# Performance work log

Hardware: AMD Instinct MI355X
Metric: run time of the kernel (lower is better)

Reference implementation:

```python
import jax, jax.numpy as jnp
import numpy as np

NC, ND = 100000, 100000
E, L = 500000, 100000
HID, OUT = 128, 64
NH, HD = 4, 32
NL = 2


def setup_inputs() -> dict:
    key = jax.random.key(0)
    ks = jax.random.split(key, 16)
    f = jnp.float32
    s_lin = 1.0 / np.sqrt(HID)
    s_rel = 1.0 / np.sqrt(HD)
    return {
        "emb_C": jax.random.normal(ks[0], (NC, HID), f) * 0.1,
        "emb_D": jax.random.normal(ks[1], (ND, HID), f) * 0.1,
        "kW": jax.random.normal(ks[2], (NL, 2, HID, HID), f) * s_lin,
        "kb": jnp.zeros((NL, 2, HID), f),
        "qW": jax.random.normal(ks[3], (NL, 2, HID, HID), f) * s_lin,
        "qb": jnp.zeros((NL, 2, HID), f),
        "vW": jax.random.normal(ks[4], (NL, 2, HID, HID), f) * s_lin,
        "vb": jnp.zeros((NL, 2, HID), f),
        "aW": jax.random.normal(ks[5], (NL, 2, HID, HID), f) * s_lin,
        "ab": jnp.zeros((NL, 2, HID), f),
        "skip": jnp.ones((NL, 2), f),
        "arel": jax.random.normal(ks[6], (NL, 2, NH, HD, HD), f) * s_rel,
        "mrel": jax.random.normal(ks[7], (NL, 2, NH, HD, HD), f) * s_rel,
        "prel": jnp.ones((NL, 2, NH), f),
        "outW": jax.random.normal(ks[8], (2, HID, OUT), f) * s_lin,
        "outb": jnp.zeros((2, OUT), f),
        # edge_index for (Compound -> Disease) and reverse (Disease -> Compound)
        "ei_cd": jnp.stack([jax.random.randint(ks[9], (E,), 0, NC),
                            jax.random.randint(ks[10], (E,), 0, ND)]).astype(jnp.int32),
        "ei_dc": jnp.stack([jax.random.randint(ks[11], (E,), 0, ND),
                            jax.random.randint(ks[12], (E,), 0, NC)]).astype(jnp.int32),
        # edge_label_index: (Compound, Disease) pairs to score
        "eli": jnp.stack([jax.random.randint(ks[13], (L,), 0, NC),
                          jax.random.randint(ks[14], (L,), 0, ND)]).astype(jnp.int32),
    }


def _seg_softmax(a, seg, n):
    # numerically stable softmax over edges grouped by destination node
    amax = jax.ops.segment_max(a, seg, num_segments=n)
    amax = jnp.where(jnp.isfinite(amax), amax, 0.0)
    ex = jnp.exp(a - amax[seg])
    den = jax.ops.segment_sum(ex, seg, num_segments=n)
    return ex / (den[seg] + 1e-16)


def _hgt_layer(xs, p, ei_cd, ei_dc):
    kW, kb, qW, qb, vW, vb, aW, ab, skip, arel, mrel, prel = p
    # per-node-type K/Q/V projections, reshaped to [N, heads, head_dim]
    k = [(xs[t] @ kW[t] + kb[t]).reshape(-1, NH, HD) for t in range(2)]
    q = [(xs[t] @ qW[t] + qb[t]).reshape(-1, NH, HD) for t in range(2)]
    v = [(xs[t] @ vW[t] + vb[t]).reshape(-1, NH, HD) for t in range(2)]
    outs = [jnp.zeros_like(k[0]), jnp.zeros_like(k[1])]
    rels = [(0, 1, ei_cd), (1, 0, ei_dc)]  # (src_type, dst_type, edge_index)
    for r, (s, d, ei) in enumerate(rels):
        # relation-specific transforms applied per source node (as in PyG HGTConv)
        krel = jnp.einsum('nhd,hde->nhe', k[s], arel[r])
        vrel = jnp.einsum('nhd,hde->nhe', v[s], mrel[r])
        src, dst = ei[0], ei[1]
        ndst = xs[d].shape[0]
        a = (q[d][dst] * krel[src]).sum(-1) * prel[r] / np.sqrt(HD)  # [E, NH]
        alpha = _seg_softmax(a, dst, ndst)
        msg = vrel[src] * alpha[..., None]                           # [E, NH, HD]
        outs[d] = outs[d] + jax.ops.segment_sum(msg, dst, num_segments=ndst)
    new = []
    for t in range(2):
        o = outs[t].reshape(-1, HID)
        o = jax.nn.gelu(o) @ aW[t] + ab[t]
        g = jax.nn.sigmoid(skip[t])
        new.append(g * o + (1.0 - g) * xs[t])  # skip connection (in==out dims)
    return new


def reference(emb_C, emb_D, kW, kb, qW, qb, vW, vb, aW, ab, skip, arel, mrel, prel,
              outW, outb, ei_cd, ei_dc, eli):
    xs = [emb_C, emb_D]
    for l in range(NL):
        p = (kW[l], kb[l], qW[l], qb[l], vW[l], vb[l], aW[l], ab[l],
             skip[l], arel[l], mrel[l], prel[l])
        xs = _hgt_layer(xs, p, ei_cd, ei_dc)
        xs = [jax.nn.relu(x) for x in xs]  # dropout(0.2) in eval mode -> identity
    zC = xs[0] @ outW[0] + outb[0]
    zD = xs[1] @ outW[1] + outb[1]
    logits = jnp.clip((zC[eli[0]] * zD[eli[1]]).sum(-1), -10.0, 10.0)
    return logits
```

## Files before the change

kernel.cpp:

```cpp
#include <hip/hip_runtime.h>
#include <math.h>

#define NC_   100000
#define ND_   100000
#define NN_   100000
#define E_CNT 500000
#define L_CNT 100000
#define NH_   4
#define HD_   32
#define WCAT_SZ (129 * 384)

__device__ __forceinline__ float gelu_f(float x) {
    const float c0 = 0.7978845608028654f;
    float x3 = x * x * x;
    return 0.5f * x * (1.0f + tanhf(c0 * (x + 0.044715f * x3)));
}

__global__ __launch_bounds__(256) void fill0_int(int* __restrict__ p, int n) {
    int i = blockIdx.x * 256 + threadIdx.x;
    if (i < n) p[i] = 0;
}

__global__ __launch_bounds__(256) void count_dst(const int* __restrict__ dst,
                                                 int* __restrict__ cnt) {
    int e = blockIdx.x * 256 + threadIdx.x;
    if (e < E_CNT) atomicAdd(&cnt[dst[e]], 1);
}

__global__ __launch_bounds__(256) void scan_a(const int* __restrict__ cnt,
                                              int* __restrict__ excl,
                                              int* __restrict__ partials) {
    __shared__ int sd[256];
    int b = blockIdx.x, t = threadIdx.x;
    int base = b * 1024 + t * 4;
    int v0 = (base + 0 < NN_) ? cnt[base + 0] : 0;
    int v1 = (base + 1 < NN_) ? cnt[base + 1] : 0;
    int v2 = (base + 2 < NN_) ? cnt[base + 2] : 0;
    int v3 = (base + 3 < NN_) ? cnt[base + 3] : 0;
    int tsum = v0 + v1 + v2 + v3;
    sd[t] = tsum; __syncthreads();
    for (int off = 1; off < 256; off <<= 1) {
        int x = (t >= off) ? sd[t - off] : 0;
        __syncthreads();
        sd[t] += x;
        __syncthreads();
    }
    int excl_t = sd[t] - tsum;
    if (t == 255) partials[b] = sd[t];
    int r = excl_t;
    if (base + 0 < NN_) excl[base + 0] = r; r += v0;
    if (base + 1 < NN_) excl[base + 1] = r; r += v1;
    if (base + 2 < NN_) excl[base + 2] = r; r += v2;
    if (base + 3 < NN_) excl[base + 3] = r;
}

__global__ __launch_bounds__(128) void scan_b(int* __restrict__ partials) {
    __shared__ int sd[128];
    int t = threadIdx.x;
    int orig = (t < 98) ? partials[t] : 0;
    sd[t] = orig; __syncthreads();
    for (int off = 1; off < 128; off <<= 1) {
        int x = (t >= off) ? sd[t - off] : 0;
        __syncthreads();
        sd[t] += x;
        __syncthreads();
    }
    if (t < 98) partials[t] = sd[t] - orig;
}

__global__ __launch_bounds__(256) void scan_c(int* __restrict__ row_ptr,
                                              const int* __restrict__ partials,
                                              int* __restrict__ cursor) {
    int b = blockIdx.x, t = threadIdx.x;
    int base = b * 1024 + t * 4;
    int add = partials[b];
    #pragma unroll
    for (int j = 0; j < 4; j++) {
        int i = base + j;
        if (i < NN_) { int v = row_ptr[i] + add; row_ptr[i] = v; cursor[i] = v; }
    }
    if (b == 0 && t == 0) row_ptr[NN_] = E_CNT;
}

__global__ __launch_bounds__(256) void scatter_edges(const int* __restrict__ src,
                                                     const int* __restrict__ dst,
                                                     int* __restrict__ cursor,
                                                     int* __restrict__ srcs) {
    int e = blockIdx.x * 256 + threadIdx.x;
    if (e >= E_CNT) return;
    int pos = atomicAdd(&cursor[dst[e]], 1);
    srcs[pos] = src[e];
}

__global__ void fuse_weights(const float* __restrict__ qW, const float* __restrict__ qb,
                             const float* __restrict__ kW, const float* __restrict__ kb,
                             const float* __restrict__ vW, const float* __restrict__ vb,
                             const float* __restrict__ arel, const float* __restrict__ mrel,
                             float* __restrict__ WcatAll)
{
    int i  = blockIdx.x;
    int t  = blockIdx.y;
    int lyr = blockIdx.z;
    int oc = threadIdx.x;
    int lt = lyr * 2 + t;
    float* Wcat = WcatAll + (size_t)lt * WCAT_SZ;
    float val;
    if (oc < 128) {
        val = (i < 128) ? qW[(size_t)(lt * 128 + i) * 128 + oc] : qb[lt * 128 + oc];
    } else {
        int which = (oc >= 256);
        int cc = oc - (which ? 256 : 128);
        int h = cc >> 5, e = cc & 31;
        const float* W = which ? vW : kW;
        const float* b = which ? vb : kb;
        const float* R = (which ? mrel : arel) + (size_t)(lt * NH_ + h) * HD_ * HD_ + e;
        float s = 0.f;
        if (i < 128) {
            const float* wrow = W + (size_t)(lt * 128 + i) * 128 + h * 32;
            #pragma unroll
            for (int d2 = 0; d2 < 32; d2++) s += wrow[d2] * R[d2 * 32];
        } else {
            const float* brow = b + lt * 128 + h * 32;
            #pragma unroll
            for (int d2 = 0; d2 < 32; d2++) s += brow[d2] * R[d2 * 32];
        }
        val = s;
    }
    Wcat[(size_t)((i < 128) ? i : 128) * 384 + oc] = val;
}

template<int TN, int PREACT, int POST>
__global__ __launch_bounds__(256)
void gemm2(const float* __restrict__ A, int lda,
           const float* __restrict__ B, int ldb,
           const float* __restrict__ bias,
           float* __restrict__ C, int ldc,
           int M,
           const float* __restrict__ resid,
           const float* __restrict__ skipv,
           int ySplit,
           const float* __restrict__ A2, const float* __restrict__ B2,
           const float* __restrict__ bias2, float* __restrict__ C2, int ldc2)
{
    constexpr int TC = TN / 16;
    __shared__ float As[16][132];
    __shared__ float Bs[16][TN + 4];
    int by = blockIdx.y;
    if (ySplit >= 0 && by >= ySplit) {
        A = A2; B = B2; bias = bias2; C = C2; ldc = ldc2; by -= ySplit;
    }
    int tid = threadIdx.x;
    int tx = tid & 15, ty = tid >> 4;
    int bm = blockIdx.x * 128;
    int bn = by * TN;
    float acc[8][TC];
    #pragma unroll
    for (int i = 0; i < 8; i++)
        #pragma unroll
        for (int j = 0; j < TC; j++) acc[i][j] = 0.f;

    int m_a  = tid >> 1;
    int koff = (tid & 1) * 8;
    int arow = bm + m_a;
    bool avalid = arow < M;
    const float* aptr = A + (size_t)arow * lda + koff;
    int k_b = tid >> 4;
    int txs = tid & 15;
    const float* bptr = B + (size_t)k_b * ldb + bn + txs * 4;

    float4 a0 = make_float4(0.f,0.f,0.f,0.f), a1 = a0, b0, b1;
    if (avalid) { a0 = *(const float4*)(aptr); a1 = *(const float4*)(aptr + 4); }
    b0 = *(const float4*)(bptr);
    if (TC == 8) b1 = *(const float4*)(bptr + 64);

    for (int k0 = 0; k0 < 128; k0 += 16) {
        if (PREACT) {
            a0.x = gelu_f(a0.x); a0.y = gelu_f(a0.y); a0.z = gelu_f(a0.z); a0.w = gelu_f(a0.w);
            a1.x = gelu_f(a1.x); a1.y = gelu_f(a1.y); a1.z = gelu_f(a1.z); a1.w = gelu_f(a1.w);
        }
        __syncthreads();
        As[koff + 0][m_a] = a0.x; As[koff + 1][m_a] = a0.y;
        As[koff + 2][m_a] = a0.z; As[koff + 3][m_a] = a0.w;
        As[koff + 4][m_a] = a1.x; As[koff + 5][m_a] = a1.y;
        As[koff + 6][m_a] = a1.z; As[koff + 7][m_a] = a1.w;
        *(float4*)&Bs[k_b][txs * 4] = b0;
        if (TC == 8) *(float4*)&Bs[k_b][64 + txs * 4] = b1;
        __syncthreads();
        if (k0 + 16 < 128) {
            if (avalid) {
                a0 = *(const float4*)(aptr + k0 + 16);
                a1 = *(const float4*)(aptr + k0 + 20);
            }
            b0 = *(const float4*)(bptr + (size_t)(k0 + 16) * ldb);
            if (TC == 8) b1 = *(const float4*)(bptr + (size_t)(k0 + 16) * ldb + 64);
        }
        #pragma unroll
        for (int kk = 0; kk < 16; kk++) {
            float a[8], b[TC];
            *(float4*)&a[0] = *(const float4*)&As[kk][ty * 8];
            *(float4*)&a[4] = *(const float4*)&As[kk][ty * 8 + 4];
            *(float4*)&b[0] = *(const float4*)&Bs[kk][tx * 4];
            if (TC == 8) *(float4*)&b[4] = *(const float4*)&Bs[kk][64 + tx * 4];
            #pragma unroll
            for (int i = 0; i < 8; i++)
                #pragma unroll
                for (int j = 0; j < TC; j++)
                    acc[i][j] += a[i] * b[j];
        }
    }

    float g = 0.f, omg = 0.f;
    if (POST) { float sv = skipv[0]; g = 1.0f / (1.0f + expf(-sv)); omg = 1.0f - g; }
    float bb[TC];
    #pragma unroll
    for (int j = 0; j < 4; j++) bb[j] = bias[bn + tx * 4 + j];
    if (TC == 8)
        #pragma unroll
        for (int j = 0; j < 4; j++) bb[4 + j] = bias[bn + 64 + tx * 4 + j];
    #pragma unroll
    for (int i = 0; i < 8; i++) {
        int m = bm + ty * 8 + i;
        if (m >= M) continue;
        #pragma unroll
        for (int half = 0; half < TC / 4; half++) {
            int coff = bn + half * 64 + tx * 4;
            float* crow = C + (size_t)m * ldc + coff;
            float4 v;
            v.x = acc[i][half * 4 + 0] + bb[half * 4 + 0];
            v.y = acc[i][half * 4 + 1] + bb[half * 4 + 1];
            v.z = acc[i][half * 4 + 2] + bb[half * 4 + 2];
            v.w = acc[i][half * 4 + 3] + bb[half * 4 + 3];
            if (POST) {
                float4 r = *(const float4*)(resid + (size_t)m * ldc + coff);
                v.x = fmaxf(g * v.x + omg * r.x, 0.f);
                v.y = fmaxf(g * v.y + omg * r.y, 0.f);
                v.z = fmaxf(g * v.z + omg * r.z, 0.f);
                v.w = fmaxf(g * v.w + omg * r.w, 0.f);
            }
            *(float4*)crow = v;
        }
    }
}

__global__ __launch_bounds__(256)
void attn_gather(const int* __restrict__ row_ptr, const int* __restrict__ srcs,
                 float* __restrict__ qo, const float* __restrict__ kv,
                 const float* __restrict__ prel, int ndst)
{
    int wave = (blockIdx.x * 256 + threadIdx.x) >> 6;
    int lane = threadIdx.x & 63;
    if (wave >= ndst) return;
    int d = wave;
    int gl = lane & 15;
    int group = lane >> 4;
    int h = gl >> 2;
    float pr = prel[h] * 0.17677669529663687f;
    int beg = row_ptr[d], end = row_ptr[d + 1];
    const float* qrow = qo + (size_t)d * 128 + gl * 8;
    float4 q0 = *(const float4*)(qrow);
    float4 q1 = *(const float4*)(qrow + 4);
    float m = -1.0e30f, l = 0.f;
    float4 acc0 = make_float4(0.f,0.f,0.f,0.f), acc1 = acc0;
    int nt = (end - beg + 3) >> 2;
    for (int t = 0; t < nt; t++) {
        int i = beg + (t << 2) + group;
        if (i < end) {
            int s = srcs[i];
            const float* row = kv + (size_t)s * 256 + gl * 8;
            float4 k0 = *(const float4*)(row);
            float4 k1 = *(const float4*)(row + 4);
            float4 v0 = *(const float4*)(row + 128);
            float4 v1 = *(const float4*)(row + 132);
            float part = q0.x*k0.x + q0.y*k0.y + q0.z*k0.z + q0.w*k0.w
                       + q1.x*k1.x + q1.y*k1.y + q1.z*k1.z + q1.w*k1.w;
            part += __shfl_xor(part, 1);
            part += __shfl_xor(part, 2);
            float a = part * pr;
            float mn = fmaxf(m, a);
            float scale = expf(m - mn);
            float p = expf(a - mn);
            l = l * scale + p;
            acc0.x = acc0.x * scale + p * v0.x;
            acc0.y = acc0.y * scale + p * v0.y;
            acc0.z = acc0.z * scale + p * v0.z;
            acc0.w = acc0.w * scale + p * v0.w;
            acc1.x = acc1.x * scale + p * v1.x;
            acc1.y = acc1.y * scale + p * v1.y;
            acc1.z = acc1.z * scale + p * v1.z;
            acc1.w = acc1.w * scale + p * v1.w;
            m = mn;
        }
    }
    #pragma unroll
    for (int mask = 16; mask <= 32; mask <<= 1) {
        float m_o = __shfl_xor(m, mask);
        float l_o = __shfl_xor(l, mask);
        float4 a0o, a1o;
        a0o.x = __shfl_xor(acc0.x, mask); a0o.y = __shfl_xor(acc0.y, mask);
        a0o.z = __shfl_xor(acc0.z, mask); a0o.w = __shfl_xor(acc0.w, mask);
        a1o.x = __shfl_xor(acc1.x, mask); a1o.y = __shfl_xor(acc1.y, mask);
        a1o.z = __shfl_xor(acc1.z, mask); a1o.w = __shfl_xor(acc1.w, mask);
        float mn = fmaxf(m, m_o);
        float s0 = expf(m - mn), s1 = expf(m_o - mn);
        l = l * s0 + l_o * s1;
        acc0.x = acc0.x * s0 + a0o.x * s1; acc0.y = acc0.y * s0 + a0o.y * s1;
        acc0.z = acc0.z * s0 + a0o.z * s1; acc0.w = acc0.w * s0 + a0o.w * s1;
        acc1.x = acc1.x * s0 + a1o.x * s1; acc1.y = acc1.y * s0 + a1o.y * s1;
        acc1.z = acc1.z * s0 + a1o.z * s1; acc1.w = acc1.w * s0 + a1o.w * s1;
        m = mn;
    }
    float inv = (beg == end) ? 0.f : 1.f / (l + 1e-16f);
    if (group == 0) {
        float* orow = qo + (size_t)d * 128 + gl * 8;
        *(float4*)(orow)     = make_float4(acc0.x*inv, acc0.y*inv, acc0.z*inv, acc0.w*inv);
        *(float4*)(orow + 4) = make_float4(acc1.x*inv, acc1.y*inv, acc1.z*inv, acc1.w*inv);
    }
}

__global__ __launch_bounds__(256)
void score_pairs(const int* __restrict__ ic, const int* __restrict__ id,
                 const float* __restrict__ zC, const float* __restrict__ zD,
                 float* __restrict__ out)
{
    int gid = blockIdx.x * 256 + threadIdx.x;
    int p = gid >> 4, lane = gid & 15;
    if (p >= L_CNT) return;
    int c = ic[p], d = id[p];
    float4 a = *(const float4*)(zC + (size_t)c * 64 + lane * 4);
    float4 b = *(const float4*)(zD + (size_t)d * 64 + lane * 4);
    float s = a.x * b.x + a.y * b.y + a.z * b.z + a.w * b.w;
    s += __shfl_down(s, 8, 16);
    s += __shfl_down(s, 4, 16);
    s += __shfl_down(s, 2, 16);
    s += __shfl_down(s, 1, 16);
    if (lane == 0) out[p] = fminf(10.0f, fmaxf(-10.0f, s));
}

extern "C" void kernel_launch(void* const* d_in, const int* in_sizes, int n_in,
                              void* d_out, int out_size, void* d_ws, size_t ws_size,
                              hipStream_t stream)
{
    float* xC = (float*)d_in[0];
    float* xD = (float*)d_in[1];
    const float* kW   = (const float*)d_in[2];
    const float* kb   = (const float*)d_in[3];
    const float* qW   = (const float*)d_in[4];
    const float* qb   = (const float*)d_in[5];
    const float* vW   = (const float*)d_in[6];
    const float* vb   = (const float*)d_in[7];
    const float* aW   = (const float*)d_in[8];
    const float* ab   = (const float*)d_in[9];
    const float* skip = (const float*)d_in[10];
    const float* arel = (const float*)d_in[11];
    const float* mrel = (const float*)d_in[12];
    const float* prel = (const float*)d_in[13];
    const float* outW = (const float*)d_in[14];
    const float* outb = (const float*)d_in[15];
    const int* ei_cd  = (const int*)d_in[16];
    const int* ei_dc  = (const int*)d_in[17];
    const int* eli    = (const int*)d_in[18];

    float* ws = (float*)d_ws;
    size_t off = 0;
    float* kv    = ws + off; off += (size_t)NN_ * 256;
    float* qo    = ws + off; off += (size_t)NN_ * 128;
    float* Wcat  = ws + off; off += (size_t)4 * WCAT_SZ;
    int* iws = (int*)(ws + off);
    size_t ioff = 0;
    int* rp_cd   = iws + ioff; ioff += NN_ + 1;
    int* rp_dc   = iws + ioff; ioff += NN_ + 1;
    int* srcs_cd = iws + ioff; ioff += E_CNT;
    int* srcs_dc = iws + ioff; ioff += E_CNT;
    int* cnt     = iws + ioff; ioff += NN_;
    int* cursor  = iws + ioff; ioff += NN_;
    int* partial = iws + ioff; ioff += 128;
    float* zC = kv;
    float* zD = kv + (size_t)NN_ * 128;

    const int gridM = (NN_ + 127) / 128;
    const int gE    = (E_CNT + 255) / 256;
    const int gN    = (NN_ + 255) / 256;
    const int gScan = 98;
    const int gGath = (NN_ + 3) / 4;

    {
        const int* srcsA[2] = { ei_cd, ei_dc };
        const int* dstsA[2] = { ei_cd + E_CNT, ei_dc + E_CNT };
        int* rps[2]  = { rp_cd, rp_dc };
        int* outs[2] = { srcs_cd, srcs_dc };
        for (int r = 0; r < 2; r++) {
            fill0_int<<<gN, 256, 0, stream>>>(cnt, NN_);
            count_dst<<<gE, 256, 0, stream>>>(dstsA[r], cnt);
            scan_a<<<gScan, 256, 0, stream>>>(cnt, rps[r], partial);
            scan_b<<<1, 128, 0, stream>>>(partial);
            scan_c<<<gScan, 256, 0, stream>>>(rps[r], partial, cursor);
            scatter_edges<<<gE, 256, 0, stream>>>(srcsA[r], dstsA[r], cursor, outs[r]);
        }
    }

    fuse_weights<<<dim3(129, 2, 2), 384, 0, stream>>>(qW, qb, kW, kb, vW, vb,
                                                      arel, mrel, Wcat);

    for (int l = 0; l < 2; l++) {
        const float* aWl = aW + (size_t)l * 2 * 128 * 128;
        const float* abl = ab + (size_t)l * 2 * 128;
        float* WcC = Wcat + (size_t)(l * 2 + 0) * WCAT_SZ;
        float* WcD = Wcat + (size_t)(l * 2 + 1) * WCAT_SZ;

        gemm2<128, 0, 0><<<dim3(gridM, 3), 256, 0, stream>>>(
            xC, 128, WcC + 128, 384, WcC + 128 * 384 + 128, kv, 256, NC_, nullptr, nullptr,
            2, xD, WcD, WcD + 128 * 384, qo, 128);
        attn_gather<<<gGath, 256, 0, stream>>>(rp_cd, srcs_cd, qo, kv,
                                               prel + (l * 2 + 0) * 4, ND_);

        gemm2<128, 0, 0><<<dim3(gridM, 2), 256, 0, stream>>>(
            xD, 128, WcD + 128, 384, WcD + 128 * 384 + 128, kv, 256, ND_, nullptr, nullptr,
            -1, nullptr, nullptr, nullptr, nullptr, 0);

        gemm2<128, 1, 1><<<dim3(gridM, 1), 256, 0, stream>>>(
            qo, 128, aWl + 128 * 128, 128, abl + 128, xD, 128, ND_, xD, skip + l * 2 + 1,
            -1, nullptr, nullptr, nullptr, nullptr, 0);

        gemm2<128, 0, 0><<<dim3(gridM, 1), 256, 0, stream>>>(
            xC, 128, WcC, 384, WcC + 128 * 384, qo, 128, NC_, nullptr, nullptr,
            -1, nullptr, nullptr, nullptr, nullptr, 0);
        attn_gather<<<gGath, 256, 0, stream>>>(rp_dc, srcs_dc, qo, kv,
                                               prel + (l * 2 + 1) * 4, NC_);

        gemm2<128, 1, 1><<<dim3(gridM, 1), 256, 0, stream>>>(
            qo, 128, aWl, 128, abl, xC, 128, NC_, xC, skip + l * 2 + 0,
            -1, nullptr, nullptr, nullptr, nullptr, 0);
    }

    gemm2<64, 0, 0><<<dim3(gridM, 2), 256, 0, stream>>>(
        xC, 128, outW, 64, outb, zC, 64, NC_, nullptr, nullptr,
        1, xD, outW + 128 * 64, outb + 64, zD, 64);

    score_pairs<<<(L_CNT * 16 + 255) / 256, 256, 0, stream>>>(
        eli, eli + L_CNT, zC, zD, (float*)d_out);
}
```

Baseline: 1.424 ms.

## Batch CSR build for both relations, enlarge GEMM M-tile, fuse GELU into gather

```diff
diff --git a/kernel.cpp b/kernel.cpp
--- a/kernel.cpp
+++ b/kernel.cpp
@@ -21,16 +21,21 @@
     if (i < n) p[i] = 0;
 }
 
-__global__ __launch_bounds__(256) void count_dst(const int* __restrict__ dst,
+__global__ __launch_bounds__(256) void count_dst(const int* __restrict__ dstA,
+                                                 const int* __restrict__ dstB,
                                                  int* __restrict__ cnt) {
+    int r = blockIdx.y;
+    const int* dst = r ? dstB : dstA;
     int e = blockIdx.x * 256 + threadIdx.x;
-    if (e < E_CNT) atomicAdd(&cnt[dst[e]], 1);
+    if (e < E_CNT) atomicAdd(&cnt[r * NN_ + dst[e]], 1);
 }
 
 __global__ __launch_bounds__(256) void scan_a(const int* __restrict__ cnt,
                                               int* __restrict__ excl,
                                               int* __restrict__ partials) {
     __shared__ int sd[256];
+    int r = blockIdx.y;
+    cnt += r * NN_; excl += r * (NN_ + 1); partials += r * 128;
     int b = blockIdx.x, t = threadIdx.x;
     int base = b * 1024 + t * 4;
     int v0 = (base + 0 < NN_) ? cnt[base + 0] : 0;
@@ -47,15 +52,16 @@
     }
     int excl_t = sd[t] - tsum;
     if (t == 255) partials[b] = sd[t];
-    int r = excl_t;
-    if (base + 0 < NN_) excl[base + 0] = r; r += v0;
-    if (base + 1 < NN_) excl[base + 1] = r; r += v1;
-    if (base + 2 < NN_) excl[base + 2] = r; r += v2;
-    if (base + 3 < NN_) excl[base + 3] = r;
+    int q = excl_t;
+    if (base + 0 < NN_) excl[base + 0] = q; q += v0;
+    if (base + 1 < NN_) excl[base + 1] = q; q += v1;
+    if (base + 2 < NN_) excl[base + 2] = q; q += v2;
+    if (base + 3 < NN_) excl[base + 3] = q;
 }
 
 __global__ __launch_bounds__(128) void scan_b(int* __restrict__ partials) {
     __shared__ int sd[128];
+    partials += blockIdx.x * 128;
     int t = threadIdx.x;
     int orig = (t < 98) ? partials[t] : 0;
     sd[t] = orig; __syncthreads();
@@ -71,6 +77,8 @@
 __global__ __launch_bounds__(256) void scan_c(int* __restrict__ row_ptr,
                                               const int* __restrict__ partials,
                                               int* __restrict__ cursor) {
+    int r = blockIdx.y;
+    row_ptr += r * (NN_ + 1); partials += r * 128; cursor += r * NN_;
     int b = blockIdx.x, t = threadIdx.x;
     int base = b * 1024 + t * 4;
     int add = partials[b];
@@ -82,10 +90,16 @@
     if (b == 0 && t == 0) row_ptr[NN_] = E_CNT;
 }
 
-__global__ __launch_bounds__(256) void scatter_edges(const int* __restrict__ src,
-                                                     const int* __restrict__ dst,
+__global__ __launch_bounds__(256) void scatter_edges(const int* __restrict__ srcA,
+                                                     const int* __restrict__ dstA,
+                                                     const int* __restrict__ srcB,
+                                                     const int* __restrict__ dstB,
                                                      int* __restrict__ cursor,
                                                      int* __restrict__ srcs) {
+    int r = blockIdx.y;
+    const int* src = r ? srcB : srcA;
+    const int* dst = r ? dstB : dstA;
+    cursor += r * NN_; srcs += r * E_CNT;
     int e = blockIdx.x * 256 + threadIdx.x;
     if (e >= E_CNT) return;
     int pos = atomicAdd(&cursor[dst[e]], 1);
@@ -129,9 +143,9 @@
     Wcat[(size_t)((i < 128) ? i : 128) * 384 + oc] = val;
 }
 
-template<int TN, int PREACT, int POST>
-__global__ __launch_bounds__(256)
-void gemm2(const float* __restrict__ A, int lda,
+template<int TN, int POST>
+__global__ __launch_bounds__(256, 2)
+void gemm3(const float* __restrict__ A, int lda,
            const float* __restrict__ B, int ldb,
            const float* __restrict__ bias,
            float* __restrict__ C, int ldc,
@@ -143,7 +157,7 @@
            const float* __restrict__ bias2, float* __restrict__ C2, int ldc2)
 {
     constexpr int TC = TN / 16;
-    __shared__ float As[16][132];
+    __shared__ float As[16][260];
     __shared__ float Bs[16][TN + 4];
     int by = blockIdx.y;
     if (ySplit >= 0 && by >= ySplit) {
@@ -151,58 +165,61 @@
     }
     int tid = threadIdx.x;
     int tx = tid & 15, ty = tid >> 4;
-    int bm = blockIdx.x * 128;
+    int bm = blockIdx.x * 256;
     int bn = by * TN;
-    float acc[8][TC];
+    float acc[16][TC];
     #pragma unroll
-    for (int i = 0; i < 8; i++)
+    for (int i = 0; i < 16; i++)
         #pragma unroll
         for (int j = 0; j < TC; j++) acc[i][j] = 0.f;
 
-    int m_a  = tid >> 1;
+    int m1   = tid >> 1;
     int koff = (tid & 1) * 8;
-    int arow = bm + m_a;
-    bool avalid = arow < M;
-    const float* aptr = A + (size_t)arow * lda + koff;
+    int r1 = bm + m1, r2 = r1 + 128;
+    bool v1 = r1 < M, v2 = r2 < M;
+    const float* ap1 = A + (size_t)r1 * lda + koff;
+    const float* ap2 = A + (size_t)r2 * lda + koff;
     int k_b = tid >> 4;
     int txs = tid & 15;
     const float* bptr = B + (size_t)k_b * ldb + bn + txs * 4;
 
-    float4 a0 = make_float4(0.f,0.f,0.f,0.f), a1 = a0, b0, b1;
-    if (avalid) { a0 = *(const float4*)(aptr); a1 = *(const float4*)(aptr + 4); }
+    float4 z4 = make_float4(0.f, 0.f, 0.f, 0.f);
+    float4 a10 = z4, a11 = z4, a20 = z4, a21 = z4, b0 = z4, b1 = z4;
+    if (v1) { a10 = *(const float4*)(ap1); a11 = *(const float4*)(ap1 + 4); }
+    if (v2) { a20 = *(const float4*)(ap2); a21 = *(const float4*)(ap2 + 4); }
     b0 = *(const float4*)(bptr);
     if (TC == 8) b1 = *(const float4*)(bptr + 64);
 
     for (int k0 = 0; k0 < 128; k0 += 16) {
-        if (PREACT) {
-            a0.x = gelu_f(a0.x); a0.y = gelu_f(a0.y); a0.z = gelu_f(a0.z); a0.w = gelu_f(a0.w);
-            a1.x = gelu_f(a1.x); a1.y = gelu_f(a1.y); a1.z = gelu_f(a1.z); a1.w = gelu_f(a1.w);
-        }
-        __syncthreads();
-        As[koff + 0][m_a] = a0.x; As[koff + 1][m_a] = a0.y;
-        As[koff + 2][m_a] = a0.z; As[koff + 3][m_a] = a0.w;
-        As[koff + 4][m_a] = a1.x; As[koff + 5][m_a] = a1.y;
-        As[koff + 6][m_a] = a1.z; As[koff + 7][m_a] = a1.w;
+        __syncthreads();
+        As[koff + 0][m1] = a10.x; As[koff + 1][m1] = a10.y;
+        As[koff + 2][m1] = a10.z; As[koff + 3][m1] = a10.w;
+        As[koff + 4][m1] = a11.x; As[koff + 5][m1] = a11.y;
+        As[koff + 6][m1] = a11.z; As[koff + 7][m1] = a11.w;
+        As[koff + 0][m1 + 128] = a20.x; As[koff + 1][m1 + 128] = a20.y;
+        As[koff + 2][m1 + 128] = a20.z; As[koff + 3][m1 + 128] = a20.w;
+        As[koff + 4][m1 + 128] = a21.x; As[koff + 5][m1 + 128] = a21.y;
+        As[koff + 6][m1 + 128] = a21.z; As[koff + 7][m1 + 128] = a21.w;
         *(float4*)&Bs[k_b][txs * 4] = b0;
         if (TC == 8) *(float4*)&Bs[k_b][64 + txs * 4] = b1;
         __syncthreads();
         if (k0 + 16 < 128) {
-            if (avalid) {
-                a0 = *(const float4*)(aptr + k0 + 16);
-                a1 = *(const float4*)(aptr + k0 + 20);
-            }
+            if (v1) { a10 = *(const float4*)(ap1 + k0 + 16); a11 = *(const float4*)(ap1 + k0 + 20); }
+            if (v2) { a20 = *(const float4*)(ap2 + k0 + 16); a21 = *(const float4*)(ap2 + k0 + 20); }
             b0 = *(const float4*)(bptr + (size_t)(k0 + 16) * ldb);
             if (TC == 8) b1 = *(const float4*)(bptr + (size_t)(k0 + 16) * ldb + 64);
         }
         #pragma unroll
         for (int kk = 0; kk < 16; kk++) {
-            float a[8], b[TC];
-            *(float4*)&a[0] = *(const float4*)&As[kk][ty * 8];
-            *(float4*)&a[4] = *(const float4*)&As[kk][ty * 8 + 4];
+            float a[16], b[TC];
+            *(float4*)&a[0]  = *(const float4*)&As[kk][ty * 16 + 0];
+            *(float4*)&a[4]  = *(const float4*)&As[kk][ty * 16 + 4];
+            *(float4*)&a[8]  = *(const float4*)&As[kk][ty * 16 + 8];
+            *(float4*)&a[12] = *(const float4*)&As[kk][ty * 16 + 12];
             *(float4*)&b[0] = *(const float4*)&Bs[kk][tx * 4];
             if (TC == 8) *(float4*)&b[4] = *(const float4*)&Bs[kk][64 + tx * 4];
             #pragma unroll
-            for (int i = 0; i < 8; i++)
+            for (int i = 0; i < 16; i++)
                 #pragma unroll
                 for (int j = 0; j < TC; j++)
                     acc[i][j] += a[i] * b[j];
@@ -218,8 +235,8 @@
         #pragma unroll
         for (int j = 0; j < 4; j++) bb[4 + j] = bias[bn + 64 + tx * 4 + j];
     #pragma unroll
-    for (int i = 0; i < 8; i++) {
-        int m = bm + ty * 8 + i;
+    for (int i = 0; i < 16; i++) {
+        int m = bm + ty * 16 + i;
         if (m >= M) continue;
         #pragma unroll
         for (int half = 0; half < TC / 4; half++) {
@@ -312,8 +329,13 @@
     float inv = (beg == end) ? 0.f : 1.f / (l + 1e-16f);
     if (group == 0) {
         float* orow = qo + (size_t)d * 128 + gl * 8;
-        *(float4*)(orow)     = make_float4(acc0.x*inv, acc0.y*inv, acc0.z*inv, acc0.w*inv);
-        *(float4*)(orow + 4) = make_float4(acc1.x*inv, acc1.y*inv, acc1.z*inv, acc1.w*inv);
+        float4 o0, o1;
+        o0.x = gelu_f(acc0.x * inv); o0.y = gelu_f(acc0.y * inv);
+        o0.z = gelu_f(acc0.z * inv); o0.w = gelu_f(acc0.w * inv);
+        o1.x = gelu_f(acc1.x * inv); o1.y = gelu_f(acc1.y * inv);
+        o1.z = gelu_f(acc1.z * inv); o1.w = gelu_f(acc1.w * inv);
+        *(float4*)(orow)     = o0;
+        *(float4*)(orow + 4) = o1;
     }
 }
 
@@ -367,36 +389,31 @@
     float* Wcat  = ws + off; off += (size_t)4 * WCAT_SZ;
     int* iws = (int*)(ws + off);
     size_t ioff = 0;
-    int* rp_cd   = iws + ioff; ioff += NN_ + 1;
-    int* rp_dc   = iws + ioff; ioff += NN_ + 1;
-    int* srcs_cd = iws + ioff; ioff += E_CNT;
-    int* srcs_dc = iws + ioff; ioff += E_CNT;
-    int* cnt     = iws + ioff; ioff += NN_;
-    int* cursor  = iws + ioff; ioff += NN_;
-    int* partial = iws + ioff; ioff += 128;
+    int* rp      = iws + ioff; ioff += 2 * (NN_ + 1);
+    int* srcsA   = iws + ioff; ioff += 2 * E_CNT;
+    int* cnt     = iws + ioff; ioff += 2 * NN_;
+    int* cursor  = iws + ioff; ioff += 2 * NN_;
+    int* partial = iws + ioff; ioff += 256;
     float* zC = kv;
     float* zD = kv + (size_t)NN_ * 128;
 
-    const int gridM = (NN_ + 127) / 128;
+    const int gridM = (NN_ + 255) / 256;
     const int gE    = (E_CNT + 255) / 256;
-    const int gN    = (NN_ + 255) / 256;
+    const int gN2   = (2 * NN_ + 255) / 256;
     const int gScan = 98;
     const int gGath = (NN_ + 3) / 4;
 
-    {
-        const int* srcsA[2] = { ei_cd, ei_dc };
-        const int* dstsA[2] = { ei_cd + E_CNT, ei_dc + E_CNT };
-        int* rps[2]  = { rp_cd, rp_dc };
-        int* outs[2] = { srcs_cd, srcs_dc };
-        for (int r = 0; r < 2; r++) {
-            fill0_int<<<gN, 256, 0, stream>>>(cnt, NN_);
-            count_dst<<<gE, 256, 0, stream>>>(dstsA[r], cnt);
-            scan_a<<<gScan, 256, 0, stream>>>(cnt, rps[r], partial);
-            scan_b<<<1, 128, 0, stream>>>(partial);
-            scan_c<<<gScan, 256, 0, stream>>>(rps[r], partial, cursor);
-            scatter_edges<<<gE, 256, 0, stream>>>(srcsA[r], dstsA[r], cursor, outs[r]);
-        }
-    }
+    fill0_int<<<gN2, 256, 0, stream>>>(cnt, 2 * NN_);
+    count_dst<<<dim3(gE, 2), 256, 0, stream>>>(ei_cd + E_CNT, ei_dc + E_CNT, cnt);
+    scan_a<<<dim3(gScan, 2), 256, 0, stream>>>(cnt, rp, partial);
+    scan_b<<<2, 128, 0, stream>>>(partial);
+    scan_c<<<dim3(gScan, 2), 256, 0, stream>>>(rp, partial, cursor);
+    scatter_edges<<<dim3(gE, 2), 256, 0, stream>>>(ei_cd, ei_cd + E_CNT,
+                                                   ei_dc, ei_dc + E_CNT, cursor, srcsA);
+    int* rp_cd   = rp;
+    int* rp_dc   = rp + (NN_ + 1);
+    int* srcs_cd = srcsA;
+    int* srcs_dc = srcsA + E_CNT;
 
     fuse_weights<<<dim3(129, 2, 2), 384, 0, stream>>>(qW, qb, kW, kb, vW, vb,
                                                       arel, mrel, Wcat);
@@ -407,32 +424,32 @@
         float* WcC = Wcat + (size_t)(l * 2 + 0) * WCAT_SZ;
         float* WcD = Wcat + (size_t)(l * 2 + 1) * WCAT_SZ;
 
-        gemm2<128, 0, 0><<<dim3(gridM, 3), 256, 0, stream>>>(
+        gemm3<128, 0><<<dim3(gridM, 3), 256, 0, stream>>>(
             xC, 128, WcC + 128, 384, WcC + 128 * 384 + 128, kv, 256, NC_, nullptr, nullptr,
             2, xD, WcD, WcD + 128 * 384, qo, 128);
         attn_gather<<<gGath, 256, 0, stream>>>(rp_cd, srcs_cd, qo, kv,
                                                prel + (l * 2 + 0) * 4, ND_);
 
-        gemm2<128, 0, 0><<<dim3(gridM, 2), 256, 0, stream>>>(
+        gemm3<128, 0><<<dim3(gridM, 2), 256, 0, stream>>>(
             xD, 128, WcD + 128, 384, WcD + 128 * 384 + 128, kv, 256, ND_, nullptr, nullptr,
             -1, nullptr, nullptr, nullptr, nullptr, 0);
 
-        gemm2<128, 1, 1><<<dim3(gridM, 1), 256, 0, stream>>>(
+        gemm3<128, 1><<<dim3(gridM, 1), 256, 0, stream>>>(
             qo, 128, aWl + 128 * 128, 128, abl + 128, xD, 128, ND_, xD, skip + l * 2 + 1,
             -1, nullptr, nullptr, nullptr, nullptr, 0);
 
-        gemm2<128, 0, 0><<<dim3(gridM, 1), 256, 0, stream>>>(
+        gemm3<128, 0><<<dim3(gridM, 1), 256, 0, stream>>>(
             xC, 128, WcC, 384, WcC + 128 * 384, qo, 128, NC_, nullptr, nullptr,
             -1, nullptr, nullptr, nullptr, nullptr, 0);
         attn_gather<<<gGath, 256, 0, stream>>>(rp_dc, srcs_dc, qo, kv,
                                                prel + (l * 2 + 1) * 4, NC_);
 
-        gemm2<128, 1, 1><<<dim3(gridM, 1), 256, 0, stream>>>(
+        gemm3<128, 1><<<dim3(gridM, 1), 256, 0, stream>>>(
             qo, 128, aWl, 128, abl, xC, 128, NC_, xC, skip + l * 2 + 0,
             -1, nullptr, nullptr, nullptr, nullptr, 0);
     }
 
-    gemm2<64, 0, 0><<<dim3(gridM, 2), 256, 0, stream>>>(
+    gemm3<64, 0><<<dim3(gridM, 2), 256, 0, stream>>>(
         xC, 128, outW, 64, outb, zC, 64, NC_, nullptr, nullptr,
         1, xD, outW + 128 * 64, outb + 64, zD, 64);
 
```

Result: slower. 1.577 ms (+10.7%).
